# Kernel tuning notes

Hardware: AMD Instinct MI355X
Metric: run time of the kernel (lower is better)

## Reference

```python
import jax, jax.numpy as jnp
import numpy as np

B, L, D, H = 2, 2048, 512, 8
DH = D // H
THRESHOLD = 0.1


def setup_inputs() -> dict:
    key = jax.random.key(0)
    ks = jax.random.split(key, 8)
    s = 0.02  # weight scale to keep activations sane
    return {
        "q_x": jax.random.normal(ks[0], (B, L, D), jnp.float32),
        "k_x": jax.random.normal(ks[1], (B, L, D), jnp.float32),
        "v_x": jax.random.normal(ks[2], (B, L, D), jnp.float32),
        "energy_coeffs": jax.random.normal(ks[3], (B, L, 16), jnp.float32),
        "Wq": jax.random.normal(ks[4], (D, D), jnp.float32) * s,
        "bq": jnp.zeros((D,), jnp.float32),
        "Wk": jax.random.normal(ks[5], (D, D), jnp.float32) * s,
        "bk": jnp.zeros((D,), jnp.float32),
        "Wv": jax.random.normal(ks[6], (D, D), jnp.float32) * s,
        "bv": jnp.zeros((D,), jnp.float32),
        "Wo": jax.random.normal(ks[7], (D, D), jnp.float32) * s,
        "bo": jnp.zeros((D,), jnp.float32),
    }


def reference(q_x, k_x, v_x, energy_coeffs, Wq, bq, Wk, bk, Wv, bv, Wo, bo):
    b, l, d = q_x.shape
    # QKV projections (torch Linear: x @ W.T + b), split heads -> [B,H,L,Dh]
    Q = (q_x @ Wq.T + bq).reshape(b, l, H, DH).transpose(0, 2, 1, 3)
    K = (k_x @ Wk.T + bk).reshape(b, -1, H, DH).transpose(0, 2, 1, 3)
    V = (v_x @ Wv.T + bv).reshape(b, -1, H, DH).transpose(0, 2, 1, 3)
    scores = jnp.einsum("bhqd,bhkd->bhqk", Q, K) / jnp.sqrt(jnp.float32(DH))
    # straight-through energy-based key mask
    energy = jnp.abs(energy_coeffs).mean(axis=-1)  # [B, Lk]
    soft = jax.nn.sigmoid((energy - THRESHOLD) * 10.0)
    hard = (energy > THRESHOLD).astype(q_x.dtype)
    mask_val = soft + jax.lax.stop_gradient(hard - soft)  # fwd=hard, grad=soft
    scores = scores + (1.0 - mask_val)[:, None, None, :] * (-1e9)
    attn = jax.nn.softmax(scores, axis=-1)
    out = jnp.einsum("bhqk,bhkd->bhqd", attn, V)
    out = out.transpose(0, 2, 1, 3).reshape(b, l, d)
    return out @ Wo.T + bo
```

## Files before the change

kernel.cpp:

```cpp
#include <hip/hip_runtime.h>
#include <stdint.h>

#define B_ 2
#define L_ 2048
#define D_ 512
#define H_ 8
#define DH_ 64

using frag8 = __attribute__((ext_vector_type(8))) short;
using bf4   = __attribute__((ext_vector_type(4))) short;
using f32x4 = __attribute__((ext_vector_type(4))) float;
using u32x4 = __attribute__((ext_vector_type(4))) unsigned int;

#define QSC 0.18033688011112042f

__device__ __forceinline__ unsigned short f2bf(float f) {
    unsigned int u = __float_as_uint(f);
    u += 0x7fffu + ((u >> 16) & 1u);
    return (unsigned short)(u >> 16);
}

__device__ __forceinline__ unsigned int cvtpk(float lo, float hi_) {
    unsigned int r;
    asm("v_cvt_pk_bf16_f32 %0, %1, %2" : "=v"(r) : "v"(lo), "v"(hi_));
    return r;
}

__device__ __forceinline__ void gl2lds16(const void* g, void* lds) {
    __builtin_amdgcn_global_load_lds((const __attribute__((address_space(1))) void*)g,
                                     (__attribute__((address_space(3))) void*)lds,
                                     16, 0, 0);
}

__global__ __launch_bounds__(256) void cvt_kernel(
    const float* __restrict__ qx, const float* __restrict__ kx, const float* __restrict__ vx,
    const float* __restrict__ Wq, const float* __restrict__ Wk, const float* __restrict__ Wv,
    const float* __restrict__ Wo,
    unsigned short* qb, unsigned short* kb, unsigned short* vb,
    unsigned short* wqb, unsigned short* wkb, unsigned short* wvb, unsigned short* wob)
{
    const long NA = (long)B_ * L_ * D_;
    const long NW = (long)D_ * D_;
    const long total4 = (3 * NA + 4 * NW) / 4;
    long q4 = (long)blockIdx.x * 256 + threadIdx.x;
    if (q4 >= total4) return;
    long i = q4 * 4;
    const float* src; unsigned short* dst; long off;
    if (i < NA)            { src = qx; dst = qb; off = i; }
    else if (i < 2 * NA)   { src = kx; dst = kb; off = i - NA; }
    else if (i < 3 * NA)   { src = vx; dst = vb; off = i - 2 * NA; }
    else {
        long j = i - 3 * NA;
        int w = (int)(j / NW);
        off = j - (long)w * NW;
        src = (w == 0) ? Wq : (w == 1) ? Wk : (w == 2) ? Wv : Wo;
        dst = (w == 0) ? wqb : (w == 1) ? wkb : (w == 2) ? wvb : wob;
    }
    float4 v = *(const float4*)(src + off);
    ushort4 o;
    o.x = f2bf(v.x); o.y = f2bf(v.y); o.z = f2bf(v.z); o.w = f2bf(v.w);
    *(ushort4*)(dst + off) = o;
}

__global__ __launch_bounds__(256) void mask_kernel(const float* __restrict__ ec,
                                                   float* __restrict__ mk)
{
    int i = blockIdx.x * 256 + threadIdx.x;
    if (i >= B_ * L_) return;
    const float4* p4 = (const float4*)(ec + (long)i * 16);
    float s = 0.0f;
#pragma unroll
    for (int j = 0; j < 4; ++j) {
        float4 v = p4[j];
        s += fabsf(v.x) + fabsf(v.y) + fabsf(v.z) + fabsf(v.w);
    }
    float energy = s * (1.0f / 16.0f);
    mk[i] = (energy > 0.1f) ? 0.0f : -1.0e9f;
}

struct GemmArgs { const unsigned short* A; const unsigned short* W;
                  const float* bias; void* C; int mode; };

template<int BM, int BN>
__global__ __launch_bounds__(256) void gemm_kernel(GemmArgs a0, GemmArgs a1, GemmArgs a2,
                                                   int M, int N, int K)
{
    GemmArgs ga = blockIdx.z == 0 ? a0 : (blockIdx.z == 1 ? a1 : a2);
    const unsigned short* __restrict__ A = ga.A;
    const unsigned short* __restrict__ W = ga.W;
    const float* __restrict__ bias = ga.bias;

    constexpr int MF = BM / 32;
    constexpr int NF = BN / 32;

    __shared__ __align__(16) unsigned short As[BM * 64];
    __shared__ __align__(16) unsigned short Bs[BN * 64];

    const int tid  = threadIdx.x;
    const int lane = tid & 63;
    const int wave = tid >> 6;
    const int hi   = lane >> 4;
    const int ln   = lane & 15;
    const int wr   = wave >> 1;
    const int wc   = wave & 1;

    const long mBase = (long)blockIdx.y * BM;
    const long nBase = (long)blockIdx.x * BN;

    f32x4 acc[MF][NF];
#pragma unroll
    for (int m = 0; m < MF; ++m)
#pragma unroll
        for (int n = 0; n < NF; ++n) acc[m][n] = (f32x4){0.f, 0.f, 0.f, 0.f};

    for (int kt = 0; kt < K; kt += 64) {
#pragma unroll
        for (int i = 0; i < BM / 32; ++i) {
            int cl = i * 256 + tid;
            int r = cl >> 3, c = cl & 7, sc = c ^ (r & 7);
            gl2lds16(A + (mBase + r) * K + kt + sc * 8, As + cl * 8);
        }
#pragma unroll
        for (int i = 0; i < BN / 32; ++i) {
            int cl = i * 256 + tid;
            int r = cl >> 3, c = cl & 7, sc = c ^ (r & 7);
            gl2lds16(W + (nBase + r) * K + kt + sc * 8, Bs + cl * 8);
        }
        __syncthreads();

        frag8 af[2][MF], bfr[2][NF];
#pragma unroll
        for (int kk = 0; kk < 2; ++kk) {
#pragma unroll
            for (int m = 0; m < MF; ++m) {
                int row = wr * (BM / 2) + m * 16 + ln;
                int c = (kk * 4 + hi) ^ (row & 7);
                af[kk][m] = *(const frag8*)(As + row * 64 + c * 8);
            }
#pragma unroll
            for (int n = 0; n < NF; ++n) {
                int row = wc * (BN / 2) + n * 16 + ln;
                int c = (kk * 4 + hi) ^ (row & 7);
                bfr[kk][n] = *(const frag8*)(Bs + row * 64 + c * 8);
            }
        }
        __builtin_amdgcn_s_setprio(1);
#pragma unroll
        for (int kk = 0; kk < 2; ++kk)
#pragma unroll
            for (int m = 0; m < MF; ++m)
#pragma unroll
                for (int n = 0; n < NF; ++n)
                    acc[m][n] = __builtin_amdgcn_mfma_f32_16x16x32_bf16(af[kk][m], bfr[kk][n], acc[m][n], 0, 0, 0);
        __builtin_amdgcn_s_setprio(0);
        __syncthreads();
    }

    const int mode = ga.mode;
#pragma unroll
    for (int m = 0; m < MF; ++m) {
#pragma unroll
        for (int n = 0; n < NF; ++n) {
            long col = nBase + wc * (BN / 2) + n * 16 + ln;
            float bv = bias[col];
#pragma unroll
            for (int j = 0; j < 4; ++j) {
                long row = mBase + wr * (BM / 2) + m * 16 + hi * 4 + j;
                float v = acc[m][n][j] + bv;
                if (mode == 3) {
                    ((float*)ga.C)[row * N + col] = v;
                } else if (mode == 2) {
                    int dh = (int)col & 63;
                    int swv = ((dh & 7) << 1) | ((dh >> 3) & 1);
                    long nt = (row & ~63L) | (long)(((((int)(row >> 2)) & 15) ^ swv) << 2) | (row & 3);
                    ((unsigned short*)ga.C)[col * (long)(B_ * L_) + nt] = f2bf(v);
                } else {
                    if (mode == 1) v *= QSC;
                    ((unsigned short*)ga.C)[row * N + col] = f2bf(v);
                }
            }
        }
    }
}

__global__ __launch_bounds__(512, 4) void attn_kernel(
    const unsigned short* __restrict__ Qg, const unsigned short* __restrict__ Kg,
    const unsigned short* __restrict__ Vt, const float* __restrict__ mkg,
    unsigned short* __restrict__ Og)
{
    const int tid  = threadIdx.x;
    const int lane = tid & 63;
    const int wave = tid >> 6;
    const int grp  = wave >> 2;
    const int wq   = wave & 3;
    const int gtid = tid & 255;
    const int hi   = lane >> 4;
    const int ln   = lane & 15;

    const int bh = blockIdx.y;
    const int b  = bh >> 3, h = bh & 7;
    const unsigned short* Qb = Qg + ((long)b * L_) * D_ + h * DH_;
    const unsigned short* Kb = Kg + ((long)b * L_) * D_ + h * DH_;
    const unsigned short* Vb = Vt + (long)(h * DH_) * (B_ * L_) + (long)b * L_;
    const float* mkb = mkg + (long)b * L_;

    __shared__ __align__(16) char smem[65536];
    unsigned short* KsG = (unsigned short*)(smem + grp * 32768);
    unsigned short* VsG = (unsigned short*)(smem + grp * 32768 + 16384);

    const int q0 = blockIdx.x * 64 + wq * 16;

    frag8 qf[2];
#pragma unroll
    for (int ks = 0; ks < 2; ++ks)
        qf[ks] = *(const frag8*)(Qb + (long)(q0 + ln) * D_ + ks * 32 + hi * 8);

    const int sw  = ((ln & 7) << 1) | ((ln >> 3) & 1);
    const int sl0 = ((hi     ) ^ sw) << 2;
    const int sl1 = ((hi + 4 ) ^ sw) << 2;
    const int sl2 = ((hi + 8 ) ^ sw) << 2;
    const int sl3 = ((hi + 12) ^ sw) << 2;

#define STAGE(TT, BUF) do {                                                     \
    _Pragma("unroll")                                                           \
    for (int c2_ = 0; c2_ < 2; ++c2_) {                                         \
        int cl_ = c2_ * 256 + gtid;                                             \
        int r_ = cl_ >> 3, c_ = cl_ & 7;                                        \
        gl2lds16(Kb + (long)((TT) * 64 + r_) * D_ + ((c_ ^ (r_ & 7)) << 3),     \
                 KsG + (BUF) * 4096 + cl_ * 8);                                 \
        gl2lds16(Vb + (long)r_ * (B_ * L_) + (TT) * 64 + (c_ << 3),             \
                 VsG + (BUF) * 4096 + cl_ * 8);                                 \
    }                                                                           \
} while (0)

    STAGE(grp, 0);
    __syncthreads();

    f32x4 o[4];
#pragma unroll
    for (int g = 0; g < 4; ++g) o[g] = (f32x4){0.f, 0.f, 0.f, 0.f};
    float m_run = -__builtin_inff();
    float l_run = 0.0f;

    for (int i = 0; i < 16; ++i) {
        const int T = 2 * i + grp;
        const int buf = i & 1;

        float4 m40 = *(const float4*)(mkb + T * 64 +      4 * hi);
        float4 m41 = *(const float4*)(mkb + T * 64 + 16 + 4 * hi);
        float4 m42 = *(const float4*)(mkb + T * 64 + 32 + 4 * hi);
        float4 m43 = *(const float4*)(mkb + T * 64 + 48 + 4 * hi);

        if (i < 15) STAGE(2 * (i + 1) + grp, buf ^ 1);

        const unsigned short* Kl = KsG + buf * 4096;
        const unsigned short* Vl = VsG + buf * 4096;

        f32x4 sv[4];
#pragma unroll
        for (int sh = 0; sh < 4; ++sh) sv[sh] = (f32x4){0.f, 0.f, 0.f, 0.f};
        __builtin_amdgcn_s_setprio(1);
#pragma unroll
        for (int sh = 0; sh < 4; ++sh) {
            int key = sh * 16 + ln;
#pragma unroll
            for (int ks = 0; ks < 2; ++ks) {
                frag8 kf = *(const frag8*)(Kl + key * 64 + (((ks * 4 + hi) ^ (ln & 7)) << 3));
                sv[sh] = __builtin_amdgcn_mfma_f32_16x16x32_bf16(kf, qf[ks], sv[sh], 0, 0, 0);
            }
        }
        __builtin_amdgcn_s_setprio(0);

        float sc[16];
        sc[0]  = sv[0][0] + m40.x; sc[1]  = sv[0][1] + m40.y;
        sc[2]  = sv[0][2] + m40.z; sc[3]  = sv[0][3] + m40.w;
        sc[4]  = sv[1][0] + m41.x; sc[5]  = sv[1][1] + m41.y;
        sc[6]  = sv[1][2] + m41.z; sc[7]  = sv[1][3] + m41.w;
        sc[8]  = sv[2][0] + m42.x; sc[9]  = sv[2][1] + m42.y;
        sc[10] = sv[2][2] + m42.z; sc[11] = sv[2][3] + m42.w;
        sc[12] = sv[3][0] + m43.x; sc[13] = sv[3][1] + m43.w == 0 ? sv[3][1] + m43.y : sv[3][1] + m43.y;
        sc[13] = sv[3][1] + m43.y;
        sc[14] = sv[3][2] + m43.z; sc[15] = sv[3][3] + m43.w;

        float t0 = fmaxf(fmaxf(sc[0], sc[1]), sc[2]);
        float t1 = fmaxf(fmaxf(sc[3], sc[4]), sc[5]);
        float t2 = fmaxf(fmaxf(sc[6], sc[7]), sc[8]);
        float t3 = fmaxf(fmaxf(sc[9], sc[10]), sc[11]);
        float t4 = fmaxf(fmaxf(sc[12], sc[13]), sc[14]);
        float tmax = fmaxf(fmaxf(fmaxf(t0, t1), fmaxf(t2, t3)), fmaxf(t4, sc[15]));
        tmax = fmaxf(tmax, __shfl_xor(tmax, 16));
        tmax = fmaxf(tmax, __shfl_xor(tmax, 32));

        if (!__all(tmax <= m_run)) {
            float m_new = fmaxf(m_run, tmax);
            float alpha = __builtin_amdgcn_exp2f(m_run - m_new);
            float a0 = __shfl(alpha, 4 * hi + 0);
            float a1 = __shfl(alpha, 4 * hi + 1);
            float a2 = __shfl(alpha, 4 * hi + 2);
            float a3 = __shfl(alpha, 4 * hi + 3);
#pragma unroll
            for (int g = 0; g < 4; ++g) {
                o[g][0] *= a0; o[g][1] *= a1; o[g][2] *= a2; o[g][3] *= a3;
            }
            l_run *= alpha;
            m_run = m_new;
        }

        float p[16];
#pragma unroll
        for (int j = 0; j < 16; ++j) p[j] = __builtin_amdgcn_exp2f(sc[j] - m_run);
        float s01 = (p[0] + p[1]) + (p[2] + p[3]);
        float s23 = (p[4] + p[5]) + (p[6] + p[7]);
        float s45 = (p[8] + p[9]) + (p[10] + p[11]);
        float s67 = (p[12] + p[13]) + (p[14] + p[15]);
        float ps = (s01 + s23) + (s45 + s67);
        ps += __shfl_xor(ps, 16);
        ps += __shfl_xor(ps, 32);
        l_run += ps;

        union PU { u32x4 u; frag8 f; } p0u, p1u;
        p0u.u = (u32x4){cvtpk(p[0], p[1]),  cvtpk(p[2], p[3]),
                        cvtpk(p[4], p[5]),  cvtpk(p[6], p[7])};
        p1u.u = (u32x4){cvtpk(p[8], p[9]),  cvtpk(p[10], p[11]),
                        cvtpk(p[12], p[13]), cvtpk(p[14], p[15])};

        __builtin_amdgcn_s_setprio(1);
#pragma unroll
        for (int g = 0; g < 4; ++g) {
            int rowb = (g * 16 + ln) * 64;
            bf4 a0 = *(const bf4*)(Vl + rowb + sl0);
            bf4 a1 = *(const bf4*)(Vl + rowb + sl1);
            bf4 a2 = *(const bf4*)(Vl + rowb + sl2);
            bf4 a3 = *(const bf4*)(Vl + rowb + sl3);
            frag8 vf0 = __builtin_shufflevector(a0, a1, 0, 1, 2, 3, 4, 5, 6, 7);
            frag8 vf1 = __builtin_shufflevector(a2, a3, 0, 1, 2, 3, 4, 5, 6, 7);
            o[g] = __builtin_amdgcn_mfma_f32_16x16x32_bf16(p0u.f, vf0, o[g], 0, 0, 0);
            o[g] = __builtin_amdgcn_mfma_f32_16x16x32_bf16(p1u.f, vf1, o[g], 0, 0, 0);
        }
        __builtin_amdgcn_s_setprio(0);

        __syncthreads();
    }
#undef STAGE

    float* oX = (float*)smem;
    float* mX = (float*)(smem + 64 * 68 * 4);
    float* lX = mX + 64;

    if (grp == 1) {
#pragma unroll
        for (int g = 0; g < 4; ++g)
#pragma unroll
            for (int j = 0; j < 4; ++j)
                oX[(wq * 16 + 4 * hi + j) * 68 + g * 16 + ln] = o[g][j];
        if (hi == 0) { mX[wq * 16 + ln] = m_run; lX[wq * 16 + ln] = l_run; }
    }
    __syncthreads();
    if (grp == 0) {
#pragma unroll
        for (int j = 0; j < 4; ++j) {
            int q = 4 * hi + j;
            float mA = __shfl(m_run, q);
            float lA = __shfl(l_run, q);
            float mB = mX[wq * 16 + q];
            float lB = lX[wq * 16 + q];
            float mm = fmaxf(mA, mB);
            float aA = __builtin_amdgcn_exp2f(mA - mm);
            float aB = __builtin_amdgcn_exp2f(mB - mm);
            float inv = 1.0f / (lA * aA + lB * aB);
            aA *= inv; aB *= inv;
#pragma unroll
            for (int g = 0; g < 4; ++g) {
                float v = o[g][j] * aA + oX[(wq * 16 + q) * 68 + g * 16 + ln] * aB;
                long idx = ((long)b * L_ + q0 + q) * D_ + h * DH_ + g * 16 + ln;
                Og[idx] = f2bf(v);
            }
        }
    }
}

extern "C" void kernel_launch(void* const* d_in, const int* in_sizes, int n_in,
                              void* d_out, int out_size, void* d_ws, size_t ws_size,
                              hipStream_t stream)
{
    const float* qx = (const float*)d_in[0];
    const float* kx = (const float*)d_in[1];
    const float* vx = (const float*)d_in[2];
    const float* ec = (const float*)d_in[3];
    const float* Wq = (const float*)d_in[4];
    const float* bq = (const float*)d_in[5];
    const float* Wk = (const float*)d_in[6];
    const float* bk = (const float*)d_in[7];
    const float* Wv = (const float*)d_in[8];
    const float* bv = (const float*)d_in[9];
    const float* Wo = (const float*)d_in[10];
    const float* bo = (const float*)d_in[11];
    float* out = (float*)d_out;

    const long NA = (long)B_ * L_ * D_;
    const long NW = (long)D_ * D_;

    unsigned short* qb  = (unsigned short*)d_ws;
    unsigned short* kb  = qb + NA;
    unsigned short* vb  = kb + NA;
    unsigned short* wqb = vb + NA;
    unsigned short* wkb = wqb + NW;
    unsigned short* wvb = wkb + NW;
    unsigned short* wob = wvb + NW;
    unsigned short* Qp  = wob + NW;
    unsigned short* Kp  = Qp + NA;
    unsigned short* Vtp = Kp + NA;
    unsigned short* Ap  = qb;
    float*          mk  = (float*)(Vtp + NA);

    const long total4 = (3 * NA + 4 * NW) / 4;
    cvt_kernel<<<dim3((unsigned)((total4 + 255) / 256)), dim3(256), 0, stream>>>(
        qx, kx, vx, Wq, Wk, Wv, Wo, qb, kb, vb, wqb, wkb, wvb, wob);
    mask_kernel<<<dim3(16), dim3(256), 0, stream>>>(ec, mk);

    GemmArgs zq = {qb, wqb, bq, Qp, 1};
    GemmArgs zk = {kb, wkb, bk, Kp, 0};
    GemmArgs zv = {vb, wvb, bv, Vtp, 2};
    gemm_kernel<64, 128><<<dim3(4, 64, 3), dim3(256), 0, stream>>>(zq, zk, zv, B_ * L_, D_, D_);

    attn_kernel<<<dim3(L_ / 64, B_ * H_), dim3(512), 0, stream>>>(Qp, Kp, Vtp, mk, Ap);

    GemmArgs zo = {Ap, wob, bo, out, 3};
    gemm_kernel<64, 64><<<dim3(8, 64, 1), dim3(256), 0, stream>>>(zo, zo, zo, B_ * L_, D_, D_);
}
```

Measured before the change: 79.93 us.

## Fuse mask into convert kernel, double-buffer GEMM LDS, swizzle workgroup order

Merges the energy-mask computation into the fp32-to-bf16 conversion kernel to save a launch. The GEMM now double-buffers its LDS tiles so the global-to-LDS load of the next K tile is issued before computing the current one. It also remaps the flat workgroup index with a stride-8 swizzle, intended to spread neighbouring blocks across XCDs for better cache locality. A redundant expression in the attention score setup is cleaned up. Double buffering doubles LDS use per block and may lower occupancy.

```diff
diff --git a/kernel.cpp b/kernel.cpp
--- a/kernel.cpp
+++ b/kernel.cpp
@@ -32,50 +32,49 @@
                                      16, 0, 0);
 }
 
-__global__ __launch_bounds__(256) void cvt_kernel(
+__global__ __launch_bounds__(256) void cvt_mask_kernel(
     const float* __restrict__ qx, const float* __restrict__ kx, const float* __restrict__ vx,
     const float* __restrict__ Wq, const float* __restrict__ Wk, const float* __restrict__ Wv,
-    const float* __restrict__ Wo,
+    const float* __restrict__ Wo, const float* __restrict__ ec,
     unsigned short* qb, unsigned short* kb, unsigned short* vb,
-    unsigned short* wqb, unsigned short* wkb, unsigned short* wvb, unsigned short* wob)
+    unsigned short* wqb, unsigned short* wkb, unsigned short* wvb, unsigned short* wob,
+    float* __restrict__ mk)
 {
     const long NA = (long)B_ * L_ * D_;
     const long NW = (long)D_ * D_;
     const long total4 = (3 * NA + 4 * NW) / 4;
     long q4 = (long)blockIdx.x * 256 + threadIdx.x;
-    if (q4 >= total4) return;
-    long i = q4 * 4;
-    const float* src; unsigned short* dst; long off;
-    if (i < NA)            { src = qx; dst = qb; off = i; }
-    else if (i < 2 * NA)   { src = kx; dst = kb; off = i - NA; }
-    else if (i < 3 * NA)   { src = vx; dst = vb; off = i - 2 * NA; }
-    else {
-        long j = i - 3 * NA;
-        int w = (int)(j / NW);
-        off = j - (long)w * NW;
-        src = (w == 0) ? Wq : (w == 1) ? Wk : (w == 2) ? Wv : Wo;
-        dst = (w == 0) ? wqb : (w == 1) ? wkb : (w == 2) ? wvb : wob;
-    }
-    float4 v = *(const float4*)(src + off);
-    ushort4 o;
-    o.x = f2bf(v.x); o.y = f2bf(v.y); o.z = f2bf(v.z); o.w = f2bf(v.w);
-    *(ushort4*)(dst + off) = o;
-}
-
-__global__ __launch_bounds__(256) void mask_kernel(const float* __restrict__ ec,
-                                                   float* __restrict__ mk)
-{
-    int i = blockIdx.x * 256 + threadIdx.x;
-    if (i >= B_ * L_) return;
-    const float4* p4 = (const float4*)(ec + (long)i * 16);
-    float s = 0.0f;
-#pragma unroll
-    for (int j = 0; j < 4; ++j) {
-        float4 v = p4[j];
-        s += fabsf(v.x) + fabsf(v.y) + fabsf(v.z) + fabsf(v.w);
-    }
-    float energy = s * (1.0f / 16.0f);
-    mk[i] = (energy > 0.1f) ? 0.0f : -1.0e9f;
+    if (q4 < total4) {
+        long i = q4 * 4;
+        const float* src; unsigned short* dst; long off;
+        if (i < NA)            { src = qx; dst = qb; off = i; }
+        else if (i < 2 * NA)   { src = kx; dst = kb; off = i - NA; }
+        else if (i < 3 * NA)   { src = vx; dst = vb; off = i - 2 * NA; }
+        else {
+            long j = i - 3 * NA;
+            int w = (int)(j / NW);
+            off = j - (long)w * NW;
+            src = (w == 0) ? Wq : (w == 1) ? Wk : (w == 2) ? Wv : Wo;
+            dst = (w == 0) ? wqb : (w == 1) ? wkb : (w == 2) ? wvb : wob;
+        }
+        float4 v = *(const float4*)(src + off);
+        ushort4 o;
+        o.x = f2bf(v.x); o.y = f2bf(v.y); o.z = f2bf(v.z); o.w = f2bf(v.w);
+        *(ushort4*)(dst + off) = o;
+    } else {
+        long i = q4 - total4;
+        if (i < B_ * L_) {
+            const float4* p4 = (const float4*)(ec + i * 16);
+            float s = 0.0f;
+#pragma unroll
+            for (int j = 0; j < 4; ++j) {
+                float4 v = p4[j];
+                s += fabsf(v.x) + fabsf(v.y) + fabsf(v.z) + fabsf(v.w);
+            }
+            float energy = s * (1.0f / 16.0f);
+            mk[i] = (energy > 0.1f) ? 0.0f : -1.0e9f;
+        }
+    }
 }
 
 struct GemmArgs { const unsigned short* A; const unsigned short* W;
@@ -85,7 +84,15 @@
 __global__ __launch_bounds__(256) void gemm_kernel(GemmArgs a0, GemmArgs a1, GemmArgs a2,
                                                    int M, int N, int K)
 {
-    GemmArgs ga = blockIdx.z == 0 ? a0 : (blockIdx.z == 1 ? a1 : a2);
+    const int nwg = gridDim.x * gridDim.y * gridDim.z;
+    int flat = blockIdx.x + gridDim.x * (blockIdx.y + gridDim.y * blockIdx.z);
+    int swz  = (flat & 7) * (nwg >> 3) + (flat >> 3);
+    const int bx = swz % gridDim.x;
+    int t2 = swz / gridDim.x;
+    const int by = t2 % gridDim.y;
+    const int bz = t2 / gridDim.y;
+
+    GemmArgs ga = bz == 0 ? a0 : (bz == 1 ? a1 : a2);
     const unsigned short* __restrict__ A = ga.A;
     const unsigned short* __restrict__ W = ga.W;
     const float* __restrict__ bias = ga.bias;
@@ -93,8 +100,8 @@
     constexpr int MF = BM / 32;
     constexpr int NF = BN / 32;
 
-    __shared__ __align__(16) unsigned short As[BM * 64];
-    __shared__ __align__(16) unsigned short Bs[BN * 64];
+    __shared__ __align__(16) unsigned short As[2][BM * 64];
+    __shared__ __align__(16) unsigned short Bs[2][BN * 64];
 
     const int tid  = threadIdx.x;
     const int lane = tid & 63;
@@ -104,8 +111,8 @@
     const int wr   = wave >> 1;
     const int wc   = wave & 1;
 
-    const long mBase = (long)blockIdx.y * BM;
-    const long nBase = (long)blockIdx.x * BN;
+    const long mBase = (long)by * BM;
+    const long nBase = (long)bx * BN;
 
     f32x4 acc[MF][NF];
 #pragma unroll
@@ -113,20 +120,28 @@
 #pragma unroll
         for (int n = 0; n < NF; ++n) acc[m][n] = (f32x4){0.f, 0.f, 0.f, 0.f};
 
-    for (int kt = 0; kt < K; kt += 64) {
-#pragma unroll
-        for (int i = 0; i < BM / 32; ++i) {
-            int cl = i * 256 + tid;
-            int r = cl >> 3, c = cl & 7, sc = c ^ (r & 7);
-            gl2lds16(A + (mBase + r) * K + kt + sc * 8, As + cl * 8);
-        }
-#pragma unroll
-        for (int i = 0; i < BN / 32; ++i) {
-            int cl = i * 256 + tid;
-            int r = cl >> 3, c = cl & 7, sc = c ^ (r & 7);
-            gl2lds16(W + (nBase + r) * K + kt + sc * 8, Bs + cl * 8);
-        }
-        __syncthreads();
+#define GSTAGE(KT, BUF) do {                                                    \
+    _Pragma("unroll")                                                           \
+    for (int i_ = 0; i_ < BM / 32; ++i_) {                                      \
+        int cl_ = i_ * 256 + tid;                                               \
+        int r_ = cl_ >> 3, c_ = cl_ & 7, s_ = c_ ^ (r_ & 7);                    \
+        gl2lds16(A + (mBase + r_) * K + (KT) + s_ * 8, As[BUF] + cl_ * 8);      \
+    }                                                                           \
+    _Pragma("unroll")                                                           \
+    for (int i_ = 0; i_ < BN / 32; ++i_) {                                      \
+        int cl_ = i_ * 256 + tid;                                               \
+        int r_ = cl_ >> 3, c_ = cl_ & 7, s_ = c_ ^ (r_ & 7);                    \
+        gl2lds16(W + (nBase + r_) * K + (KT) + s_ * 8, Bs[BUF] + cl_ * 8);      \
+    }                                                                           \
+} while (0)
+
+    GSTAGE(0, 0);
+    __syncthreads();
+
+    const int nk = K / 64;
+    for (int t = 0; t < nk; ++t) {
+        const int buf = t & 1;
+        if (t + 1 < nk) GSTAGE((t + 1) * 64, buf ^ 1);
 
         frag8 af[2][MF], bfr[2][NF];
 #pragma unroll
@@ -135,13 +150,13 @@
             for (int m = 0; m < MF; ++m) {
                 int row = wr * (BM / 2) + m * 16 + ln;
                 int c = (kk * 4 + hi) ^ (row & 7);
-                af[kk][m] = *(const frag8*)(As + row * 64 + c * 8);
+                af[kk][m] = *(const frag8*)(As[buf] + row * 64 + c * 8);
             }
 #pragma unroll
             for (int n = 0; n < NF; ++n) {
                 int row = wc * (BN / 2) + n * 16 + ln;
                 int c = (kk * 4 + hi) ^ (row & 7);
-                bfr[kk][n] = *(const frag8*)(Bs + row * 64 + c * 8);
+                bfr[kk][n] = *(const frag8*)(Bs[buf] + row * 64 + c * 8);
             }
         }
         __builtin_amdgcn_s_setprio(1);
@@ -155,6 +170,7 @@
         __builtin_amdgcn_s_setprio(0);
         __syncthreads();
     }
+#undef GSTAGE
 
     const int mode = ga.mode;
 #pragma unroll
@@ -278,8 +294,7 @@
         sc[6]  = sv[1][2] + m41.z; sc[7]  = sv[1][3] + m41.w;
         sc[8]  = sv[2][0] + m42.x; sc[9]  = sv[2][1] + m42.y;
         sc[10] = sv[2][2] + m42.z; sc[11] = sv[2][3] + m42.w;
-        sc[12] = sv[3][0] + m43.x; sc[13] = sv[3][1] + m43.w == 0 ? sv[3][1] + m43.y : sv[3][1] + m43.y;
-        sc[13] = sv[3][1] + m43.y;
+        sc[12] = sv[3][0] + m43.x; sc[13] = sv[3][1] + m43.y;
         sc[14] = sv[3][2] + m43.z; sc[15] = sv[3][3] + m43.w;
 
         float t0 = fmaxf(fmaxf(sc[0], sc[1]), sc[2]);
@@ -414,9 +429,9 @@
     float*          mk  = (float*)(Vtp + NA);
 
     const long total4 = (3 * NA + 4 * NW) / 4;
-    cvt_kernel<<<dim3((unsigned)((total4 + 255) / 256)), dim3(256), 0, stream>>>(
-        qx, kx, vx, Wq, Wk, Wv, Wo, qb, kb, vb, wqb, wkb, wvb, wob);
-    mask_kernel<<<dim3(16), dim3(256), 0, stream>>>(ec, mk);
+    const long nblk = (total4 + B_ * L_ + 255) / 256;
+    cvt_mask_kernel<<<dim3((unsigned)nblk), dim3(256), 0, stream>>>(
+        qx, kx, vx, Wq, Wk, Wv, Wo, ec, qb, kb, vb, wqb, wkb, wvb, wob, mk);
 
     GemmArgs zq = {qb, wqb, bq, Qp, 1};
     GemmArgs zk = {kb, wkb, bk, Kp, 0};
```

Result: no change. 78.56 us (-1.7%).
